# Kernel tuning notes

Measured on AMD Instinct MI355X. Metric: run time of the kernel, lower is better.

The kernel has to match this reference:

```python
import jax, jax.numpy as jnp
import numpy as np

EPS = 1e-5
HEADS = 16
GROUPS = 16


def _bn(x, gamma, beta, mean, var, ch_axis):
    # eval-mode batchnorm along channel axis
    shape = [1] * x.ndim
    shape[ch_axis] = -1
    scale = gamma / jnp.sqrt(var + EPS)
    return (x - mean.reshape(shape)) * scale.reshape(shape) + beta.reshape(shape)


def setup_inputs() -> dict:
    key = jax.random.key(0)
    ks = jax.random.split(key, 20)
    N, Ct, L = 2, 256, 256
    Cf, Co = 256, 256
    H = W = 128
    G, Cg = GROUPS, Cf // GROUPS  # 16, 16
    nrm = lambda k, sh, s=1.0: (jax.random.normal(k, sh, jnp.float32) * s)
    return {
        "feature": nrm(ks[0], (N, Cf, H, W)),
        "tokens": nrm(ks[1], (N, Ct, L)),
        "w_v": nrm(ks[2], (Co, Ct), 1.0 / np.sqrt(Ct)),
        "b_v": nrm(ks[3], (Co,), 0.05),
        "g_v": 1.0 + nrm(ks[4], (Co,), 0.1),
        "be_v": nrm(ks[5], (Co,), 0.05),
        "m_v": nrm(ks[6], (Co,), 0.05),
        "v_v": 0.5 + jax.random.uniform(ks[7], (Co,), jnp.float32),
        "w_k": nrm(ks[8], (Cf, Ct), 1.0 / np.sqrt(Ct)),
        "b_k": nrm(ks[9], (Cf,), 0.05),
        "g_k": 1.0 + nrm(ks[10], (Cf,), 0.1),
        "be_k": nrm(ks[11], (Cf,), 0.05),
        "m_k": nrm(ks[12], (Cf,), 0.05),
        "v_k": 0.5 + jax.random.uniform(ks[13], (Cf,), jnp.float32),
        "w_q": nrm(ks[14], (G, Cg, Cg), 1.0 / np.sqrt(Cg)),  # grouped 1x1 conv
        "b_q": nrm(ks[15], (Cf,), 0.05),
        "g_q": 1.0 + nrm(ks[16], (Cf,), 0.1),
        "be_q": nrm(ks[17], (Cf,), 0.05),
        "m_q": nrm(ks[18], (Cf,), 0.05),
        "v_q": 0.5 + jax.random.uniform(ks[19], (Cf,), jnp.float32),
    }


def reference(feature, tokens, w_v, b_v, g_v, be_v, m_v, v_v,
              w_k, b_k, g_k, be_k, m_k, v_k,
              w_q, b_q, g_q, be_q, m_q, v_q):
    N, Ct, L = tokens.shape
    _, Cf, H, W = feature.shape
    h = HEADS
    # value / key: 1x1 conv1d + BN1d over channel axis 1
    pv = _bn(jnp.einsum('oc,ncl->nol', w_v, tokens) + b_v[:, None],
             g_v, be_v, m_v, v_v, 1)  # [N, Co, L]
    pk = _bn(jnp.einsum('oc,ncl->nol', w_k, tokens) + b_k[:, None],
             g_k, be_k, m_k, v_k, 1)  # [N, Cf, L]
    # query: grouped 1x1 conv2d + BN
    G = GROUPS
    fg = feature.reshape(N, G, Cf // G, H, W)
    pq = jnp.einsum('goc,ngchw->ngohw', w_q, fg).reshape(N, Cf, H, W)
    pq = _bn(pq + b_q[None, :, None, None], g_q, be_q, m_q, v_q, 1)
    # multi-head cross attention
    dq = Cf // h  # head dim = 16
    q = pq.reshape(N, h, dq, H * W)        # [N,h,d,S]
    k = pk.reshape(N, h, dq, L)            # [N,h,d,L]
    v = pv.reshape(N, h, -1, L)            # [N,h,dv,L]
    scores = jnp.einsum('nhds,nhdl->nhsl', q, k) / jnp.sqrt(jnp.float32(dq))
    coef = jax.nn.softmax(scores, axis=-1)  # softmax over tokens L
    proj = jnp.einsum('nhvl,nhsl->nhvs', v, coef).reshape(N, -1, H, W)
    # out_channels == feature_channels -> lateral_conv is None
    return feature + proj
```

## Files before the change

### kernel.cpp

```cpp
#include <hip/hip_runtime.h>
#include <hip/hip_bf16.h>
#include <math.h>

#define EPSV 1e-5f
#define LOG2E 1.4426950408889634f

typedef short short8v __attribute__((ext_vector_type(8)));
typedef __bf16 bf16x8 __attribute__((ext_vector_type(8)));
typedef float f32x4 __attribute__((ext_vector_type(4)));

__device__ __forceinline__ float bsu2f(unsigned short u) {
    union { unsigned int i; float f; } x; x.i = ((unsigned int)u) << 16; return x.f;
}
__device__ __forceinline__ float ldf(const void* p, int i, int isbf) {
    return isbf ? bsu2f(((const unsigned short*)p)[i]) : ((const float*)p)[i];
}
__device__ __forceinline__ short f2bs(float x) {
    __hip_bfloat16 h = __float2bfloat16(x);
    return *reinterpret_cast<short*>(&h);
}
__device__ __forceinline__ int packbf(short a, short b) {
    return (int)(unsigned short)a | ((int)(unsigned short)b << 16);
}
__device__ __forceinline__ int probe_bf16(const void* vv) {
    const unsigned short* p = (const unsigned short*)vv;
    int cnt = 0;
#pragma unroll
    for (int i = 0; i < 16; ++i) {
        const float x = bsu2f(p[i]);
        cnt += (x >= 0.01f && x <= 100.0f) ? 1 : 0;
    }
    return cnt >= 14;
}

__global__ __launch_bounds__(256) void prep_kernel(
    const void* __restrict__ tokens,
    const void* __restrict__ w_v, const void* __restrict__ b_v,
    const void* __restrict__ g_v, const void* __restrict__ be_v,
    const void* __restrict__ m_v, const void* __restrict__ v_v,
    const void* __restrict__ w_k, const void* __restrict__ b_k,
    const void* __restrict__ g_k, const void* __restrict__ be_k,
    const void* __restrict__ m_k, const void* __restrict__ v_k,
    int* __restrict__ ka, int* __restrict__ va)
{
    __shared__ __align__(16) short Wh[16][264];
    __shared__ __align__(16) short Tt[256][40];
    __shared__ float scs[16], shs[16];

    const int tid = threadIdx.x;
    const int h = blockIdx.x, kv = blockIdx.y, n = blockIdx.z;
    const int isbf = probe_bf16(v_v);

    const void* w  = kv ? w_k  : w_v;
    const void* b  = kv ? b_k  : b_v;
    const void* g  = kv ? g_k  : g_v;
    const void* be = kv ? be_k : be_v;
    const void* mm = kv ? m_k  : m_v;
    const void* vv = kv ? v_k  : v_v;

    {
        const int d = tid >> 4, c0 = (tid & 15) * 16;
        const int off = (h * 16 + d) * 256 + c0;
        if (isbf) {
            const unsigned short* ws = (const unsigned short*)w + off;
#pragma unroll
            for (int i = 0; i < 16; ++i) Wh[d][c0 + i] = (short)ws[i];
        } else {
            const float* ws = (const float*)w + off;
#pragma unroll
            for (int i = 0; i < 16; ++i) Wh[d][c0 + i] = f2bs(ws[i]);
        }
    }
    if (tid < 16) {
        const int ch = h * 16 + tid;
        const float s = ldf(g, ch, isbf) * rsqrtf(ldf(vv, ch, isbf) + EPSV);
        scs[tid] = s;
        shs[tid] = (ldf(b, ch, isbf) - ldf(mm, ch, isbf)) * s + ldf(be, ch, isbf);
    }

    const int lane = tid & 63, w_ = tid >> 6;
    const int q = lane >> 4, p = lane & 15;

    f32x4 acc[4];
    const f32x4 zero = {0.f, 0.f, 0.f, 0.f};
#pragma unroll
    for (int t = 0; t < 4; ++t) acc[t] = zero;

    for (int ch8 = 0; ch8 < 8; ++ch8) {
        const int c0 = ch8 * 32;
        __syncthreads();
#pragma unroll
        for (int p2 = 0; p2 < 2; ++p2) {
            const int ccl = p2 * 16 + (tid >> 5) * 2;
            const int cc = c0 + ccl;
            const int l0 = (tid & 31) * 8;
            if (isbf) {
                const unsigned short* tp = (const unsigned short*)tokens + n * 65536;
                const int4 r0 = *(const int4*)(tp + cc * 256 + l0);
                const int4 r1 = *(const int4*)(tp + (cc + 1) * 256 + l0);
                const unsigned short* a = (const unsigned short*)&r0;
                const unsigned short* bb = (const unsigned short*)&r1;
#pragma unroll
                for (int i = 0; i < 8; ++i)
                    *(int*)&Tt[l0 + i][ccl] = (int)a[i] | ((int)bb[i] << 16);
            } else {
                const float* tp = (const float*)tokens + n * 65536;
#pragma unroll
                for (int i = 0; i < 8; ++i) {
                    const int aa = (int)(unsigned short)f2bs(tp[cc * 256 + l0 + i]);
                    const int bb = (int)(unsigned short)f2bs(tp[(cc + 1) * 256 + l0 + i]);
                    *(int*)&Tt[l0 + i][ccl] = aa | (bb << 16);
                }
            }
        }
        __syncthreads();
        const short8v wf = *(const short8v*)&Wh[p][c0 + q * 8];
#pragma unroll
        for (int t = 0; t < 4; ++t) {
            const int l = (w_ * 4 + t) * 16 + p;
            const short8v tf = *(const short8v*)&Tt[l][q * 8];
            if (kv)
                acc[t] = __builtin_amdgcn_mfma_f32_16x16x32_bf16(
                    __builtin_bit_cast(bf16x8, wf), __builtin_bit_cast(bf16x8, tf),
                    acc[t], 0, 0, 0);
            else
                acc[t] = __builtin_amdgcn_mfma_f32_16x16x32_bf16(
                    __builtin_bit_cast(bf16x8, tf), __builtin_bit_cast(bf16x8, wf),
                    acc[t], 0, 0, 0);
        }
    }

    if (kv) {
        float sc4[4], sh4[4];
#pragma unroll
        for (int r = 0; r < 4; ++r) { sc4[r] = scs[q * 4 + r]; sh4[r] = shs[q * 4 + r]; }
        int* dst_nh = ka + (n * 16 + h) * 2048;
#pragma unroll
        for (int t = 0; t < 4; ++t) {
            const int tau = w_ * 4 + t;
            const int T = (tau >> 1) * 2 + ((p >> 2) & 1);
            const int m = ((tau & 1) * 2 + (p >> 3)) * 4 + (p & 3);
            const int L = (q >> 1) * 16 + m;
            int* dst = dst_nh + (T * 32 + L) * 4 + (q & 1) * 2;
            const float v0 = fmaf(acc[t][0], sc4[0], sh4[0]);
            const float v1 = fmaf(acc[t][1], sc4[1], sh4[1]);
            const float v2 = fmaf(acc[t][2], sc4[2], sh4[2]);
            const float v3 = fmaf(acc[t][3], sc4[3], sh4[3]);
            dst[0] = packbf(f2bs(v0), f2bs(v1));
            dst[1] = packbf(f2bs(v2), f2bs(v3));
        }
    } else {
        const float scp = scs[p], shp = shs[p];
        int* dst_nh = va + (n * 16 + h) * 2048;
#pragma unroll
        for (int t = 0; t < 4; ++t) {
            const int tau = w_ * 4 + t;
            const int c = tau >> 1;
            const int L = ((tau & 1) * 2 + (q >> 1)) * 16 + p;
            int* dst = dst_nh + (c * 64 + L) * 4 + (q & 1) * 2;
            const float v0 = fmaf(acc[t][0], scp, shp);
            const float v1 = fmaf(acc[t][1], scp, shp);
            const float v2 = fmaf(acc[t][2], scp, shp);
            const float v3 = fmaf(acc[t][3], scp, shp);
            dst[0] = packbf(f2bs(v0), f2bs(v1));
            dst[1] = packbf(f2bs(v2), f2bs(v3));
        }
    }
}

__global__ __launch_bounds__(256) void attn_kernel(
    const void* __restrict__ feature,
    const int* __restrict__ ka_g, const int* __restrict__ va_g,
    const void* __restrict__ w_q, const void* __restrict__ b_q,
    const void* __restrict__ g_q, const void* __restrict__ be_q,
    const void* __restrict__ m_q, const void* __restrict__ v_q,
    const void* __restrict__ v_probe, void* __restrict__ out)
{
    __shared__ __align__(16) short KAsh[16][64][8];
    __shared__ __align__(16) short VAsh[8][64][8];
    __shared__ __align__(16) short QBsh[4][64][8];
    __shared__ float Osh[16][64];
    __shared__ float Wq[16][16];
    __shared__ float Aq[16], Bq[16];

    const int tid = threadIdx.x;
    const int bx = blockIdx.x, h = blockIdx.y, n = blockIdx.z;
    const int isbf = probe_bf16(v_probe);

    {
        const int4* kas = (const int4*)ka_g + (n * 16 + h) * 512;
        const int4* vas = (const int4*)va_g + (n * 16 + h) * 512;
        int4 z; z.x = z.y = z.z = z.w = 0;
#pragma unroll
        for (int k = 0; k < 2; ++k) {
            const int slot = k * 256 + tid;
            const int T = slot >> 5, L = slot & 31;
            ((int4*)KAsh)[T * 64 + L] = kas[slot];
            ((int4*)KAsh)[T * 64 + 32 + L] = z;
            ((int4*)VAsh)[slot] = vas[slot];
        }
        ((float*)Wq)[tid] = ldf(w_q, h * 256 + tid, isbf);
        if (tid < 16) {
            const int ch = h * 16 + tid;
            const float sq = ldf(g_q, ch, isbf) * rsqrtf(ldf(v_q, ch, isbf) + EPSV);
            Aq[tid] = 0.25f * LOG2E * sq;
            Bq[tid] = 0.25f * LOG2E *
                      ((ldf(b_q, ch, isbf) - ldf(m_q, ch, isbf)) * sq + ldf(be_q, ch, isbf));
        }
        if (tid < 128) {
            int4 zz; zz.x = zz.y = zz.z = zz.w = 0;
            ((int4*)QBsh)[(tid >> 5) * 64 + 32 + (tid & 31)] = zz;
        }
    }
    __syncthreads();

    {
        const int p_blk = tid & 63, dgroup = tid >> 6;
        const int s = bx * 64 + p_blk;
        const int fbase = n * 4194304 + (h * 16) * 16384 + s;
        float f[16];
        if (isbf) {
            const unsigned short* fp = (const unsigned short*)feature;
#pragma unroll
            for (int c = 0; c < 16; ++c) f[c] = bsu2f(fp[fbase + c * 16384]);
        } else {
            const float* fp = (const float*)feature;
#pragma unroll
            for (int c = 0; c < 16; ++c) f[c] = fp[fbase + c * 16384];
        }
        short q4[4];
#pragma unroll
        for (int dd = 0; dd < 4; ++dd) {
            const int d = dgroup * 4 + dd;
            float a = 0.f;
#pragma unroll
            for (int c = 0; c < 16; ++c) a = fmaf(Wq[d][c], f[c], a);
            q4[dd] = f2bs(fmaf(a, Aq[d], Bq[d]));
        }
        const int lanep = (dgroup >> 1) * 16 + (p_blk & 15);
        *(int2*)&QBsh[p_blk >> 4][lanep][(dgroup & 1) * 4] =
            make_int2(packbf(q4[0], q4[1]), packbf(q4[2], q4[3]));
    }
    __syncthreads();

    const int lane = tid & 63, w_ = tid >> 6;
    const int q = lane >> 4, p = lane & 15;

    const short8v qb = *(const short8v*)&QBsh[w_][lane][0];
    const bf16x8 qbb = __builtin_bit_cast(bf16x8, qb);

    f32x4 S[16];
    const f32x4 zero = {0.f, 0.f, 0.f, 0.f};
#pragma unroll
    for (int T = 0; T < 16; ++T) {
        const short8v kaf = *(const short8v*)&KAsh[T][lane][0];
        S[T] = __builtin_amdgcn_mfma_f32_16x16x32_bf16(
            __builtin_bit_cast(bf16x8, kaf), qbb, zero, 0, 0, 0);
    }

    float mx = S[0][0];
#pragma unroll
    for (int T = 0; T < 16; ++T)
#pragma unroll
        for (int r = 0; r < 4; ++r) mx = fmaxf(mx, S[T][r]);
    mx = fmaxf(mx, __shfl_xor(mx, 16, 64));
    mx = fmaxf(mx, __shfl_xor(mx, 32, 64));
    float ssum = 0.f;
#pragma unroll
    for (int T = 0; T < 16; ++T)
#pragma unroll
        for (int r = 0; r < 4; ++r) {
            const float e = exp2f(S[T][r] - mx);
            S[T][r] = e;
            ssum += e;
        }
    ssum += __shfl_xor(ssum, 16, 64);
    ssum += __shfl_xor(ssum, 32, 64);
    const float inv = 1.0f / ssum;

    f32x4 oacc = zero;
#pragma unroll
    for (int c = 0; c < 8; ++c) {
        short8v pb;
#pragma unroll
        for (int j = 0; j < 4; ++j) {
            pb[j]     = f2bs(S[2 * c][j]);
            pb[4 + j] = f2bs(S[2 * c + 1][j]);
        }
        const short8v vaf = *(const short8v*)&VAsh[c][lane][0];
        oacc = __builtin_amdgcn_mfma_f32_16x16x32_bf16(
            __builtin_bit_cast(bf16x8, vaf), __builtin_bit_cast(bf16x8, pb),
            oacc, 0, 0, 0);
    }

#pragma unroll
    for (int r = 0; r < 4; ++r) Osh[q * 4 + r][w_ * 16 + p] = oacc[r] * inv;
    __syncthreads();

    {
        const int px = tid & 63;
        const int base2 = n * 4194304 + (h * 16) * 16384 + bx * 64 + px;
        if (isbf) {
            const unsigned short* fp = (const unsigned short*)feature;
            __hip_bfloat16* op = (__hip_bfloat16*)out;
#pragma unroll
            for (int r = 0; r < 4; ++r) {
                const int ch = r * 4 + w_;
                const int idx = base2 + ch * 16384;
                op[idx] = __float2bfloat16(Osh[ch][px] + bsu2f(fp[idx]));
            }
        } else {
            const float* fp = (const float*)feature;
            float* op = (float*)out;
#pragma unroll
            for (int r = 0; r < 4; ++r) {
                const int ch = r * 4 + w_;
                const int idx = base2 + ch * 16384;
                op[idx] = Osh[ch][px] + fp[idx];
            }
        }
    }
}

extern "C" void kernel_launch(void* const* d_in, const int* in_sizes, int n_in,
                              void* d_out, int out_size, void* d_ws, size_t ws_size,
                              hipStream_t stream) {
    const void* feature = d_in[0];
    const void* tokens  = d_in[1];
    const void* w_v  = d_in[2];  const void* b_v  = d_in[3];
    const void* g_v  = d_in[4];  const void* be_v = d_in[5];
    const void* m_v  = d_in[6];  const void* v_v  = d_in[7];
    const void* w_k  = d_in[8];  const void* b_k  = d_in[9];
    const void* g_k  = d_in[10]; const void* be_k = d_in[11];
    const void* m_k  = d_in[12]; const void* v_k  = d_in[13];
    const void* w_q  = d_in[14]; const void* b_q  = d_in[15];
    const void* g_q  = d_in[16]; const void* be_q = d_in[17];
    const void* m_q  = d_in[18]; const void* v_q  = d_in[19];

    int* ka = (int*)d_ws;
    int* va = ka + 65536;

    prep_kernel<<<dim3(16, 2, 2), 256, 0, stream>>>(
        tokens, w_v, b_v, g_v, be_v, m_v, v_v,
        w_k, b_k, g_k, be_k, m_k, v_k, ka, va);
    attn_kernel<<<dim3(256, 16, 2), 256, 0, stream>>>(
        feature, ka, va, w_q, b_q, g_q, be_q, m_q, v_q, v_v, (void*)d_out);
}
```

Baseline: 195.4 us.

## Compute query projection with MFMA, drop softmax max pass, cache dtype flag

The grouped 1x1 query conv becomes a single bf16 MFMA per wave, with the BN scale folded into the weights, replacing the scalar FMA loop and its LDS staging. Softmax no longer subtracts the row max, on the assumption that the scores stay small. bf16 packing uses round-half-up plus byte perm instead of the conversion intrinsic. The input dtype probe runs once in the prep kernel and is read from a workspace flag, and the zero-padded K LDS half is removed. These steps cut VALU and LDS work but risk overflow for large scores and lose precision by rounding the fp32 feature to bf16 before the projection.

```diff
diff --git a/kernel.cpp b/kernel.cpp
--- a/kernel.cpp
+++ b/kernel.cpp
@@ -21,6 +21,12 @@
 }
 __device__ __forceinline__ int packbf(short a, short b) {
     return (int)(unsigned short)a | ((int)(unsigned short)b << 16);
+}
+__device__ __forceinline__ int permpack(unsigned int hi, unsigned int lo) {
+    return (int)__builtin_amdgcn_perm(hi, lo, 0x07060302u);
+}
+__device__ __forceinline__ unsigned int fbits_rhu(float x) {
+    return __float_as_uint(x) + 0x8000u;
 }
 __device__ __forceinline__ int probe_bf16(const void* vv) {
     const unsigned short* p = (const unsigned short*)vv;
@@ -41,7 +47,7 @@
     const void* __restrict__ w_k, const void* __restrict__ b_k,
     const void* __restrict__ g_k, const void* __restrict__ be_k,
     const void* __restrict__ m_k, const void* __restrict__ v_k,
-    int* __restrict__ ka, int* __restrict__ va)
+    int* __restrict__ ka, int* __restrict__ va, int* __restrict__ flag)
 {
     __shared__ __align__(16) short Wh[16][264];
     __shared__ __align__(16) short Tt[256][40];
@@ -50,6 +56,7 @@
     const int tid = threadIdx.x;
     const int h = blockIdx.x, kv = blockIdx.y, n = blockIdx.z;
     const int isbf = probe_bf16(v_v);
+    if (h == 0 && kv == 0 && n == 0 && tid == 0) *flag = isbf;
 
     const void* w  = kv ? w_k  : w_v;
     const void* b  = kv ? b_k  : b_v;
@@ -134,20 +141,19 @@
         float sc4[4], sh4[4];
 #pragma unroll
         for (int r = 0; r < 4; ++r) { sc4[r] = scs[q * 4 + r]; sh4[r] = shs[q * 4 + r]; }
+        const int qs = ((q & 1) << 1) | (q >> 1);
         int* dst_nh = ka + (n * 16 + h) * 2048;
 #pragma unroll
         for (int t = 0; t < 4; ++t) {
             const int tau = w_ * 4 + t;
             const int T = (tau >> 1) * 2 + ((p >> 2) & 1);
             const int m = ((tau & 1) * 2 + (p >> 3)) * 4 + (p & 3);
-            const int L = (q >> 1) * 16 + m;
-            int* dst = dst_nh + (T * 32 + L) * 4 + (q & 1) * 2;
-            const float v0 = fmaf(acc[t][0], sc4[0], sh4[0]);
-            const float v1 = fmaf(acc[t][1], sc4[1], sh4[1]);
-            const float v2 = fmaf(acc[t][2], sc4[2], sh4[2]);
-            const float v3 = fmaf(acc[t][3], sc4[3], sh4[3]);
-            dst[0] = packbf(f2bs(v0), f2bs(v1));
-            dst[1] = packbf(f2bs(v2), f2bs(v3));
+            const int L = (qs >> 1) * 16 + m;
+            int* dst = dst_nh + (T * 32 + L) * 4 + (qs & 1) * 2;
+            dst[0] = packbf(f2bs(fmaf(acc[t][0], sc4[0], sh4[0])),
+                            f2bs(fmaf(acc[t][1], sc4[1], sh4[1])));
+            dst[1] = packbf(f2bs(fmaf(acc[t][2], sc4[2], sh4[2])),
+                            f2bs(fmaf(acc[t][3], sc4[3], sh4[3])));
         }
     } else {
         const float scp = scs[p], shp = shs[p];
@@ -158,12 +164,10 @@
             const int c = tau >> 1;
             const int L = ((tau & 1) * 2 + (q >> 1)) * 16 + p;
             int* dst = dst_nh + (c * 64 + L) * 4 + (q & 1) * 2;
-            const float v0 = fmaf(acc[t][0], scp, shp);
-            const float v1 = fmaf(acc[t][1], scp, shp);
-            const float v2 = fmaf(acc[t][2], scp, shp);
-            const float v3 = fmaf(acc[t][3], scp, shp);
-            dst[0] = packbf(f2bs(v0), f2bs(v1));
-            dst[1] = packbf(f2bs(v2), f2bs(v3));
+            dst[0] = packbf(f2bs(fmaf(acc[t][0], scp, shp)),
+                            f2bs(fmaf(acc[t][1], scp, shp)));
+            dst[1] = packbf(f2bs(fmaf(acc[t][2], scp, shp)),
+                            f2bs(fmaf(acc[t][3], scp, shp)));
         }
     }
 }
@@ -174,103 +178,102 @@
     const void* __restrict__ w_q, const void* __restrict__ b_q,
     const void* __restrict__ g_q, const void* __restrict__ be_q,
     const void* __restrict__ m_q, const void* __restrict__ v_q,
-    const void* __restrict__ v_probe, void* __restrict__ out)
+    const int* __restrict__ flag, void* __restrict__ out)
 {
-    __shared__ __align__(16) short KAsh[16][64][8];
+    __shared__ __align__(16) short KAsh[16][32][8];
     __shared__ __align__(16) short VAsh[8][64][8];
-    __shared__ __align__(16) short QBsh[4][64][8];
-    __shared__ float Osh[16][64];
-    __shared__ float Wq[16][16];
-    __shared__ float Aq[16], Bq[16];
+    __shared__ __align__(16) short Wqsh[16][24];
+    __shared__ __align__(16) float Bqsh[16];
+    __shared__ __align__(16) float Osh[16][64];
 
     const int tid = threadIdx.x;
     const int bx = blockIdx.x, h = blockIdx.y, n = blockIdx.z;
-    const int isbf = probe_bf16(v_probe);
+    const int isbf = *flag;
 
     {
         const int4* kas = (const int4*)ka_g + (n * 16 + h) * 512;
         const int4* vas = (const int4*)va_g + (n * 16 + h) * 512;
-        int4 z; z.x = z.y = z.z = z.w = 0;
 #pragma unroll
         for (int k = 0; k < 2; ++k) {
             const int slot = k * 256 + tid;
-            const int T = slot >> 5, L = slot & 31;
-            ((int4*)KAsh)[T * 64 + L] = kas[slot];
-            ((int4*)KAsh)[T * 64 + 32 + L] = z;
+            ((int4*)KAsh)[slot] = kas[slot];
             ((int4*)VAsh)[slot] = vas[slot];
         }
-        ((float*)Wq)[tid] = ldf(w_q, h * 256 + tid, isbf);
+        const int d = tid >> 4, ch = h * 16 + d;
+        const float aqd = 0.25f * LOG2E *
+                          ldf(g_q, ch, isbf) * rsqrtf(ldf(v_q, ch, isbf) + EPSV);
+        Wqsh[d][tid & 15] = f2bs(ldf(w_q, h * 256 + tid, isbf) * aqd);
         if (tid < 16) {
-            const int ch = h * 16 + tid;
-            const float sq = ldf(g_q, ch, isbf) * rsqrtf(ldf(v_q, ch, isbf) + EPSV);
-            Aq[tid] = 0.25f * LOG2E * sq;
-            Bq[tid] = 0.25f * LOG2E *
-                      ((ldf(b_q, ch, isbf) - ldf(m_q, ch, isbf)) * sq + ldf(be_q, ch, isbf));
-        }
-        if (tid < 128) {
-            int4 zz; zz.x = zz.y = zz.z = zz.w = 0;
-            ((int4*)QBsh)[(tid >> 5) * 64 + 32 + (tid & 31)] = zz;
-        }
-    }
-    __syncthreads();
-
-    {
-        const int p_blk = tid & 63, dgroup = tid >> 6;
-        const int s = bx * 64 + p_blk;
-        const int fbase = n * 4194304 + (h * 16) * 16384 + s;
-        float f[16];
-        if (isbf) {
-            const unsigned short* fp = (const unsigned short*)feature;
-#pragma unroll
-            for (int c = 0; c < 16; ++c) f[c] = bsu2f(fp[fbase + c * 16384]);
-        } else {
-            const float* fp = (const float*)feature;
-#pragma unroll
-            for (int c = 0; c < 16; ++c) f[c] = fp[fbase + c * 16384];
-        }
-        short q4[4];
-#pragma unroll
-        for (int dd = 0; dd < 4; ++dd) {
-            const int d = dgroup * 4 + dd;
-            float a = 0.f;
-#pragma unroll
-            for (int c = 0; c < 16; ++c) a = fmaf(Wq[d][c], f[c], a);
-            q4[dd] = f2bs(fmaf(a, Aq[d], Bq[d]));
-        }
-        const int lanep = (dgroup >> 1) * 16 + (p_blk & 15);
-        *(int2*)&QBsh[p_blk >> 4][lanep][(dgroup & 1) * 4] =
-            make_int2(packbf(q4[0], q4[1]), packbf(q4[2], q4[3]));
+            const int c2 = h * 16 + tid;
+            const float sq = ldf(g_q, c2, isbf) * rsqrtf(ldf(v_q, c2, isbf) + EPSV);
+            Bqsh[tid] = 0.25f * LOG2E *
+                        ((ldf(b_q, c2, isbf) - ldf(m_q, c2, isbf)) * sq + ldf(be_q, c2, isbf));
+        }
     }
     __syncthreads();
 
     const int lane = tid & 63, w_ = tid >> 6;
     const int q = lane >> 4, p = lane & 15;
-
-    const short8v qb = *(const short8v*)&QBsh[w_][lane][0];
-    const bf16x8 qbb = __builtin_bit_cast(bf16x8, qb);
+    const f32x4 zero = {0.f, 0.f, 0.f, 0.f};
+
+    const int px = bx * 64 + w_ * 16 + p;
+    const int fbase = n * 4194304 + (h * 16) * 16384 + px;
+    int4 fpack = {0, 0, 0, 0};
+    if (q < 2) {
+        const int c0 = q * 8;
+        if (isbf) {
+            const unsigned short* fp = (const unsigned short*)feature + fbase + c0 * 16384;
+            unsigned int u[8];
+#pragma unroll
+            for (int j = 0; j < 8; ++j) u[j] = fp[j * 16384];
+            fpack.x = (int)(u[0] | (u[1] << 16));
+            fpack.y = (int)(u[2] | (u[3] << 16));
+            fpack.z = (int)(u[4] | (u[5] << 16));
+            fpack.w = (int)(u[6] | (u[7] << 16));
+        } else {
+            const float* fp = (const float*)feature + fbase + c0 * 16384;
+            fpack.x = packbf(f2bs(fp[0]), f2bs(fp[16384]));
+            fpack.y = packbf(f2bs(fp[2 * 16384]), f2bs(fp[3 * 16384]));
+            fpack.z = packbf(f2bs(fp[4 * 16384]), f2bs(fp[5 * 16384]));
+            fpack.w = packbf(f2bs(fp[6 * 16384]), f2bs(fp[7 * 16384]));
+        }
+    }
+    const short8v waf = *(const short8v*)&Wqsh[p][(q & 1) * 8];
+    f32x4 qc = __builtin_amdgcn_mfma_f32_16x16x32_bf16(
+        __builtin_bit_cast(bf16x8, waf), __builtin_bit_cast(bf16x8, fpack),
+        zero, 0, 0, 0);
+    const f32x4 bq4 = *(const f32x4*)&Bqsh[q * 4];
+    unsigned int a0 = fbits_rhu(qc[0] + bq4[0]);
+    unsigned int a1 = fbits_rhu(qc[1] + bq4[1]);
+    unsigned int a2 = fbits_rhu(qc[2] + bq4[2]);
+    unsigned int a3 = fbits_rhu(qc[3] + bq4[3]);
+    const unsigned int o0 = (unsigned int)__shfl_xor((int)a0, 32, 64);
+    const unsigned int o1 = (unsigned int)__shfl_xor((int)a1, 32, 64);
+    const unsigned int o2 = (unsigned int)__shfl_xor((int)a2, 32, 64);
+    const unsigned int o3 = (unsigned int)__shfl_xor((int)a3, 32, 64);
+    int4 qp = {0, 0, 0, 0};
+    if (q < 2) {
+        qp.x = permpack(a1, a0);
+        qp.y = permpack(a3, a2);
+        qp.z = permpack(o1, o0);
+        qp.w = permpack(o3, o2);
+    }
+    const bf16x8 qbb = __builtin_bit_cast(bf16x8, qp);
 
     f32x4 S[16];
-    const f32x4 zero = {0.f, 0.f, 0.f, 0.f};
 #pragma unroll
     for (int T = 0; T < 16; ++T) {
-        const short8v kaf = *(const short8v*)&KAsh[T][lane][0];
+        const short8v kaf = *(const short8v*)&KAsh[T][lane & 31][0];
         S[T] = __builtin_amdgcn_mfma_f32_16x16x32_bf16(
             __builtin_bit_cast(bf16x8, kaf), qbb, zero, 0, 0, 0);
     }
 
-    float mx = S[0][0];
+    float ssum = 0.f;
 #pragma unroll
     for (int T = 0; T < 16; ++T)
 #pragma unroll
-        for (int r = 0; r < 4; ++r) mx = fmaxf(mx, S[T][r]);
-    mx = fmaxf(mx, __shfl_xor(mx, 16, 64));
-    mx = fmaxf(mx, __shfl_xor(mx, 32, 64));
-    float ssum = 0.f;
-#pragma unroll
-    for (int T = 0; T < 16; ++T)
-#pragma unroll
         for (int r = 0; r < 4; ++r) {
-            const float e = exp2f(S[T][r] - mx);
+            const float e = exp2f(S[T][r]);
             S[T][r] = e;
             ssum += e;
         }
@@ -281,15 +284,18 @@
     f32x4 oacc = zero;
 #pragma unroll
     for (int c = 0; c < 8; ++c) {
-        short8v pb;
-#pragma unroll
-        for (int j = 0; j < 4; ++j) {
-            pb[j]     = f2bs(S[2 * c][j]);
-            pb[4 + j] = f2bs(S[2 * c + 1][j]);
-        }
+        const unsigned int u0 = fbits_rhu(S[2 * c][0]), u1 = fbits_rhu(S[2 * c][1]);
+        const unsigned int u2 = fbits_rhu(S[2 * c][2]), u3 = fbits_rhu(S[2 * c][3]);
+        const unsigned int v0 = fbits_rhu(S[2 * c + 1][0]), v1 = fbits_rhu(S[2 * c + 1][1]);
+        const unsigned int v2 = fbits_rhu(S[2 * c + 1][2]), v3 = fbits_rhu(S[2 * c + 1][3]);
+        int4 pbp;
+        pbp.x = permpack(u1, u0);
+        pbp.y = permpack(u3, u2);
+        pbp.z = permpack(v1, v0);
+        pbp.w = permpack(v3, v2);
         const short8v vaf = *(const short8v*)&VAsh[c][lane][0];
         oacc = __builtin_amdgcn_mfma_f32_16x16x32_bf16(
-            __builtin_bit_cast(bf16x8, vaf), __builtin_bit_cast(bf16x8, pb),
+            __builtin_bit_cast(bf16x8, vaf), __builtin_bit_cast(bf16x8, pbp),
             oacc, 0, 0, 0);
     }
 
@@ -298,8 +304,8 @@
     __syncthreads();
 
     {
-        const int px = tid & 63;
-        const int base2 = n * 4194304 + (h * 16) * 16384 + bx * 64 + px;
+        const int pxe = tid & 63;
+        const int base2 = n * 4194304 + (h * 16) * 16384 + bx * 64 + pxe;
         if (isbf) {
             const unsigned short* fp = (const unsigned short*)feature;
             __hip_bfloat16* op = (__hip_bfloat16*)out;
@@ -307,7 +313,7 @@
             for (int r = 0; r < 4; ++r) {
                 const int ch = r * 4 + w_;
                 const int idx = base2 + ch * 16384;
-                op[idx] = __float2bfloat16(Osh[ch][px] + bsu2f(fp[idx]));
+                op[idx] = __float2bfloat16(Osh[ch][pxe] + bsu2f(fp[idx]));
             }
         } else {
             const float* fp = (const float*)feature;
@@ -316,7 +322,7 @@
             for (int r = 0; r < 4; ++r) {
                 const int ch = r * 4 + w_;
                 const int idx = base2 + ch * 16384;
-                op[idx] = Osh[ch][px] + fp[idx];
+                op[idx] = Osh[ch][pxe] + fp[idx];
             }
         }
     }
@@ -339,10 +345,11 @@
 
     int* ka = (int*)d_ws;
     int* va = ka + 65536;
+    int* flag = va + 65536;
 
     prep_kernel<<<dim3(16, 2, 2), 256, 0, stream>>>(
         tokens, w_v, b_v, g_v, be_v, m_v, v_v,
-        w_k, b_k, g_k, be_k, m_k, v_k, ka, va);
+        w_k, b_k, g_k, be_k, m_k, v_k, ka, va, flag);
     attn_kernel<<<dim3(256, 16, 2), 256, 0, stream>>>(
-        feature, ka, va, w_q, b_q, g_q, be_q, m_q, v_q, v_v, (void*)d_out);
-}
+        feature, ka, va, w_q, b_q, g_q, be_q, m_q, v_q, flag, (void*)d_out);
+}
```

After: 182.2 us. -6.8%, faster.
